# Kernel tuning notes

Measured on AMD Instinct MI355X. Metric: run time of the kernel, lower is better.

Reference implementation:

```python
import jax, jax.numpy as jnp
import numpy as np

B, S, H = 16, 1024, 1024
MAX_SIMS = 100
K_FOCUS = 3  # min(3, seq_len)
SIM_OPTIONS = jnp.array([10, 25, 50, 75, 100], dtype=jnp.int32)


def _gelu(x):
    return jax.nn.gelu(x, approximate=False)  # torch nn.GELU default = exact erf


def _mlp(x, W1, b1, W2, b2):
    return _gelu(x @ W1 + b1) @ W2 + b2


def setup_inputs() -> dict:
    key = jax.random.key(0)
    ks = jax.random.split(key, 24)
    sc = 0.02
    d = {
        'hidden_states': jax.random.normal(ks[0], (B, S, H), dtype=jnp.float32),
        'attention_mask': jnp.ones((B, S), dtype=jnp.int32),
        # simulation_controller: Linear(H,H) -> GELU -> Linear(H,5)
        'Wsc1': jax.random.normal(ks[1], (H, H)) * sc, 'bsc1': jnp.zeros((H,)),
        'Wsc2': jax.random.normal(ks[2], (H, 5)) * sc, 'bsc2': jnp.zeros((5,)),
        # policy: Linear(H,H) -> GELU -> Linear(H,H)
        'Wp1': jax.random.normal(ks[3], (H, H)) * sc, 'bp1': jnp.zeros((H,)),
        'Wp2': jax.random.normal(ks[4], (H, H)) * sc, 'bp2': jnp.zeros((H,)),
        # transition: Linear(2H,H) -> GELU -> (Dropout eval=identity) -> Linear(H,H)
        'Wt1': jax.random.normal(ks[5], (2 * H, H)) * sc, 'bt1': jnp.zeros((H,)),
        'Wt2': jax.random.normal(ks[6], (H, H)) * sc, 'bt2': jnp.zeros((H,)),
        # action_value: Linear(2H,H) -> GELU -> Linear(H,1)
        'Wav1': jax.random.normal(ks[7], (2 * H, H)) * sc, 'bav1': jnp.zeros((H,)),
        'Wav2': jax.random.normal(ks[8], (H, 1)) * sc, 'bav2': jnp.zeros((1,)),
        # aggregation: Linear(2H,H) -> GELU -> Linear(H,H)
        'Wg1': jax.random.normal(ks[9], (2 * H, H)) * sc, 'bg1': jnp.zeros((H,)),
        'Wg2': jax.random.normal(ks[10], (H, H)) * sc, 'bg2': jnp.zeros((H,)),
    }
    return d


def reference(hidden_states, attention_mask,
              Wsc1, bsc1, Wsc2, bsc2,
              Wp1, bp1, Wp2, bp2,
              Wt1, bt1, Wt2, bt2,
              Wav1, bav1, Wav2, bav2,
              Wg1, bg1, Wg2, bg2):
    b, s, h = hidden_states.shape
    root = hidden_states
    # eval-mode sim count selection: argmax over controller logits
    sim_logits = _mlp(root[:, 0], Wsc1, bsc1, Wsc2, bsc2)          # [B,5]
    sims = SIM_OPTIONS[jnp.argmax(sim_logits, axis=-1)]            # [B]

    policy_scores = _mlp(root, Wp1, bp1, Wp2, bp2)                 # [B,S,H]
    focus_logits = policy_scores.mean(axis=-1)                     # [B,S]
    focus_logits = jnp.where(attention_mask == 0, -1e9, focus_logits)
    root_mean = root.mean(axis=1)                                  # [B,H]
    brange = jnp.arange(b)
    base_key = jax.random.key(42)

    def step(acc, t):
        k = jax.random.fold_in(base_key, t)
        # multinomial without replacement via Gumbel top-k on the logits
        g = jax.random.gumbel(k, (b, s), dtype=focus_logits.dtype)
        _, focus_pos = jax.lax.top_k(focus_logits + g, K_FOCUS)    # [B,3]
        focus_states = jnp.take_along_axis(root, focus_pos[:, :, None], axis=1)  # [B,3,H]
        current = root
        for j in range(K_FOCUS):
            trans_in = jnp.concatenate([current.mean(axis=1), focus_states[:, j]], axis=-1)  # [B,2H]
            new_state = _mlp(trans_in, Wt1, bt1, Wt2, bt2)         # [B,H]
            current = current.at[brange, focus_pos[:, j]].set(new_state)
        value = _mlp(jnp.concatenate([root_mean, current.mean(axis=1)], axis=-1),
                     Wav1, bav1, Wav2, bav2)                       # [B,1]
        w = jax.nn.sigmoid(value)[:, :, None]                      # [B,1,1]
        active = (t < sims).astype(current.dtype)[:, None, None]   # mask sims beyond per-example count
        return acc + active * w * current, None

    acc, _ = jax.lax.scan(step, root, jnp.arange(MAX_SIMS))
    enhanced = _mlp(jnp.concatenate([root, acc], axis=-1), Wg1, bg1, Wg2, bg2)
    return hidden_states + enhanced
```

## Files before the change

kernel.cpp:

```cpp
#include <hip/hip_runtime.h>
#include <hip/hip_bf16.h>
#include <cstdint>
#include <math.h>


#define SEQ 1024
#define BATCH 16
#define HDIM 1024
#define NSIM 100
#define NCHAIN (NSIM * BATCH)
#define NCH3 (3 * NCHAIN)
#define SHC (SEQ * HDIM)

typedef short bf16x8 __attribute__((ext_vector_type(8)));
typedef float f32x4 __attribute__((ext_vector_type(4)));
typedef float float4v __attribute__((ext_vector_type(4)));

__device__ __forceinline__ unsigned short f2bf(float f) {
    union { float f; uint32_t u; } c; c.f = f;
    uint32_t u = c.u;
    return (unsigned short)((u + 0x7FFFu + ((u >> 16) & 1u)) >> 16);
}
__device__ __forceinline__ float bf2f(unsigned short h) {
    union { uint32_t u; float f; } c; c.u = ((uint32_t)h) << 16;
    return c.f;
}

__device__ __forceinline__ void gll16(const void* g, void* l) {
    __builtin_amdgcn_global_load_lds(
        (const __attribute__((address_space(1))) void*)g,
        (__attribute__((address_space(3))) void*)l, 16, 0, 0);
}

__device__ __forceinline__ float gelu32(float x) {
    return 0.5f * x * (1.0f + erff(x * 0.70710678f));
}

__device__ __forceinline__ void swz_block(int& bx, int& by) {
    int gx = gridDim.x;
    int h = blockIdx.y * gx + blockIdx.x;
    int nwg = gx * gridDim.y;
    int l = (h & 7) * (nwg >> 3) + (h >> 3);
    bx = l % gx; by = l / gx;
}

__device__ __forceinline__ uint32_t rotl32(uint32_t v, int r) {
    return (v << r) | (v >> (32 - r));
}

__device__ __forceinline__ void threefry(uint32_t k0, uint32_t k1,
                                         uint32_t c0, uint32_t c1,
                                         uint32_t& o0, uint32_t& o1) {
    uint32_t ks0 = k0, ks1 = k1, ks2 = k0 ^ k1 ^ 0x1BD11BDAu;
    uint32_t x0 = c0 + ks0, x1 = c1 + ks1;
#define TFR(r) { x0 += x1; x1 = rotl32(x1, r); x1 ^= x0; }
    TFR(13) TFR(15) TFR(26) TFR(6)   x0 += ks1; x1 += ks2 + 1u;
    TFR(17) TFR(29) TFR(16) TFR(24)  x0 += ks2; x1 += ks0 + 2u;
    TFR(13) TFR(15) TFR(26) TFR(6)   x0 += ks0; x1 += ks1 + 3u;
    TFR(17) TFR(29) TFR(16) TFR(24)  x0 += ks1; x1 += ks2 + 4u;
    TFR(13) TFR(15) TFR(26) TFR(6)   x0 += ks2; x1 += ks0 + 5u;
#undef TFR
    o0 = x0; o1 = x1;
}

__device__ __forceinline__ bool better(float va, int ia, float vb, int ib) {
    return (va > vb) || (va == vb && ia < ib);
}

__global__ __launch_bounds__(256)
void transpose_bf16(const float* __restrict__ W, unsigned short* __restrict__ WT,
                    int K, int N) {
    __shared__ float t[32][33];
    int kb = blockIdx.x * 32, nb = blockIdx.y * 32;
    int tx = threadIdx.x & 31, ty4 = threadIdx.x >> 5;
#pragma unroll
    for (int p = 0; p < 4; ++p) {
        int ky = ty4 + p * 8;
        t[ky][tx] = W[(long)(kb + ky) * N + nb + tx];
    }
    __syncthreads();
#pragma unroll
    for (int p = 0; p < 4; ++p) {
        int ny = ty4 + p * 8;
        WT[(long)(nb + ny) * K + kb + tx] = f2bf(t[tx][ny]);
    }
}

__global__ __launch_bounds__(256)
void transpose_split3(const float* __restrict__ W, unsigned short* __restrict__ WT3,
                      int K, int N) {
    __shared__ float t[32][33];
    int kb = blockIdx.x * 32, nb = blockIdx.y * 32;
    int tx = threadIdx.x & 31, ty4 = threadIdx.x >> 5;
#pragma unroll
    for (int p = 0; p < 4; ++p) {
        int ky = ty4 + p * 8;
        t[ky][tx] = W[(long)(kb + ky) * N + nb + tx];
    }
    __syncthreads();
#pragma unroll
    for (int p = 0; p < 4; ++p) {
        int ny = ty4 + p * 8;
        float w = t[tx][ny];
        unsigned short h = f2bf(w);
        unsigned short l = f2bf(w - bf2f(h));
        long base = (long)(nb + ny) * 3072;
        WT3[base + kb + tx] = h;
        WT3[base + 1024 + kb + tx] = l;
        WT3[base + 2048 + kb + tx] = h;
    }
}

__global__ __launch_bounds__(256)
void cvt_split(const float* __restrict__ src, unsigned short* __restrict__ hi,
               unsigned short* __restrict__ lo, long n8) {
    long i = (long)blockIdx.x * 256 + threadIdx.x;
    long stride = (long)gridDim.x * 256;
    for (; i < n8; i += stride) {
        const float* s = src + i * 8;
        float4v v0 = *(const float4v*)s;
        float4v v1 = *(const float4v*)(s + 4);
        bf16x8 h, l;
#pragma unroll
        for (int e = 0; e < 4; ++e) {
            unsigned short h0 = f2bf(v0[e]);
            h[e] = (short)h0;
            unsigned short h1 = f2bf(v1[e]);
            h[e + 4] = (short)h1;
            if (lo) {
                l[e] = (short)f2bf(v0[e] - bf2f(h0));
                l[e + 4] = (short)f2bf(v1[e] - bf2f(h1));
            }
        }
        *(bf16x8*)&hi[i * 8] = h;
        if (lo) *(bf16x8*)&lo[i * 8] = l;
    }
}

__global__ __launch_bounds__(256)
void rv2_kernel(const float* __restrict__ rmean, const float* __restrict__ W,
                float* __restrict__ Rv) {
    int blk = blockIdx.x;
    int b = blk >> 5, nc = (blk >> 3) & 3, kc = blk & 7;
    int n = (nc << 8) + threadIdx.x;
    float s = 0.f;
    int k0 = kc << 7;
    for (int k = k0; k < k0 + 128; ++k)
        s = fmaf(rmean[b * 1024 + k], W[(long)k * 1024 + n], s);
    atomicAdd(&Rv[b * 1024 + n], s);
}

__global__ __launch_bounds__(256)
void rootmean_part(const float* __restrict__ root, double* __restrict__ part) {
    int b = blockIdx.x >> 4, sc = blockIdx.x & 15;
#pragma unroll
    for (int hp = 0; hp < 4; ++hp) {
        int h = (hp << 8) + threadIdx.x;
        const float* base = root + (size_t)b * SHC + ((size_t)sc << 16) + h;
        double s = 0.0;
        for (int ss = 0; ss < 64; ++ss) s += (double)base[(size_t)ss << 10];
        part[(((long)b << 4) + sc) * 1024 + h] = s;
    }
}
__global__ void rootmean_fin(const double* __restrict__ part, float* __restrict__ rmean,
                             unsigned short* __restrict__ rmean_bf) {
    int e = blockIdx.x * 256 + threadIdx.x;
    int b = e >> 10, h = e & 1023;
    double s = 0.0;
    for (int sc = 0; sc < 16; ++sc) s += part[(((long)b << 4) + sc) * 1024 + h];
    float v = (float)(s * (1.0 / 1024.0));
    rmean[e] = v;
    rmean_bf[e] = f2bf(v);
}

template<int TM, int TN, int BK, int EPI>
__global__ __launch_bounds__(512)
void gemm_bt(const unsigned short* __restrict__ Av1, long lda1, const int* __restrict__ a1rows,
             const unsigned short* __restrict__ Av2, long lda2, const int* __restrict__ a2rows,
             int K1, int kmod1,
             const unsigned short* __restrict__ WT,
             const float* __restrict__ bias,
             const float* __restrict__ wp2m, double* __restrict__ fl64,
             const float* __restrict__ Pre,
             const float* __restrict__ Cadd,
             float* __restrict__ C,
             unsigned short* __restrict__ Cbf,
             long ldc, int M, int N, int K, int doGelu) {
    constexpr int MT = TM / 32;
    constexpr int NT = TN / 64;
    constexpr int WROWS = TM / 2;
    constexpr int WCOLS = TN / 4;
    constexpr int CH = BK / 8;
    constexpr int ASLOT = TM * CH;
    constexpr int BSLOT = TN * CH;
    __shared__ unsigned short As[2][TM * BK];
    __shared__ unsigned short Bs[2][TN * BK];
    __shared__ int r1s[TM], r2s[TM];
    int tid = threadIdx.x;
    int bx, by; swz_block(bx, by);
    int row0 = by * TM, col0 = bx * TN;
    if (tid < TM) {
        int gm = row0 + tid; if (gm >= M) gm = M - 1;
        r1s[tid] = a1rows ? a1rows[gm] : gm;
        r2s[tid] = a2rows ? a2rows[gm] : gm;
    }
    int wid = tid >> 6, lane = tid & 63;
    int wr = wid >> 2, wc = wid & 3;
    int llo = lane & 15, lhi = lane >> 4;
    auto swzc = [](int cs, int r) -> int {
        if constexpr (BK == 64) return cs ^ (r & 7);
        else                    return cs ^ ((r >> 1) & 3);
    };
    f32x4 acc[MT][NT];
#pragma unroll
    for (int i = 0; i < MT; i++)
#pragma unroll
        for (int j = 0; j < NT; j++) acc[i][j] = (f32x4){0.f, 0.f, 0.f, 0.f};
    __syncthreads();

    auto stage = [&](int k0, int b) {
#pragma unroll
        for (int i = 0; i < (BSLOT + 511) / 512; ++i) {
            int q = tid + (i << 9);
            if (BSLOT % 512 == 0 || q < BSLOT) {
                int r = q / CH, cs = q % CH, c = swzc(cs, r);
                gll16(WT + (long)(col0 + r) * K + (k0 + (c << 3)),
                      (char*)Bs[b] + (q << 4));
            }
        }
        bool s1 = (k0 < K1);
        const unsigned short* Ab = s1 ? Av1 : Av2;
        const int* rsel = s1 ? r1s : r2s;
        long lda = s1 ? lda1 : lda2;
        int kb = s1 ? (k0 & kmod1) : (k0 - K1);
#pragma unroll
        for (int i = 0; i < (ASLOT + 511) / 512; ++i) {
            int q = tid + (i << 9);
            if (ASLOT % 512 == 0 || q < ASLOT) {
                int r = q / CH, cs = q % CH, c = swzc(cs, r);
                gll16(Ab + (long)rsel[r] * lda + (kb + (c << 3)),
                      (char*)As[b] + (q << 4));
            }
        }
    };

    stage(0, 0);
    int nIt = K / BK;
    for (int it = 0; it < nIt; ++it) {
        int cur = it & 1;
        __syncthreads();
        if (it + 1 < nIt) stage((it + 1) * BK, cur ^ 1);
        __builtin_amdgcn_sched_barrier(0);
        char* AsB = (char*)As[cur];
        char* BsB = (char*)Bs[cur];
#pragma unroll
        for (int ks = 0; ks < BK / 32; ++ks) {
            bf16x8 af[MT], bfv[NT];
#pragma unroll
            for (int mt = 0; mt < MT; ++mt) {
                int r = wr * WROWS + mt * 16 + llo;
                int pc = swzc((ks << 2) | lhi, r);
                af[mt] = *(const bf16x8*)(AsB + ((r * CH + pc) << 4));
            }
#pragma unroll
            for (int nt = 0; nt < NT; ++nt) {
                int r = wc * WCOLS + nt * 16 + llo;
                int pc = swzc((ks << 2) | lhi, r);
                bfv[nt] = *(const bf16x8*)(BsB + ((r * CH + pc) << 4));
            }
#pragma unroll
            for (int mt = 0; mt < MT; ++mt)
#pragma unroll
                for (int nt = 0; nt < NT; ++nt)
                    acc[mt][nt] = __builtin_amdgcn_mfma_f32_16x16x32_bf16(
                        af[mt], bfv[nt], acc[mt][nt], 0, 0, 0);
        }
    }
    if constexpr (EPI == 0) {
#pragma unroll
        for (int mt = 0; mt < MT; ++mt) {
#pragma unroll
            for (int nt = 0; nt < NT; ++nt) {
                int gn = col0 + wc * WCOLS + nt * 16 + llo;
#pragma unroll
                for (int r = 0; r < 4; ++r) {
                    int rl = wr * WROWS + mt * 16 + lhi * 4 + r;
                    int gm = row0 + rl;
                    if (gm >= M) continue;
                    float v = acc[mt][nt][r] + bias[gn];
                    if (Pre) v += Pre[(long)r2s[rl] * 1024 + gn];
                    if (doGelu) v = gelu32(v);
                    if (Cadd) v += Cadd[(long)gm * ldc + gn];
                    if (C)   C[(long)gm * ldc + gn] = v;
                    if (Cbf) Cbf[(long)gm * ldc + gn] = f2bf(v);
                }
            }
        }
    } else {
#pragma unroll
        for (int mt = 0; mt < MT; ++mt) {
            double part[4] = {0.0, 0.0, 0.0, 0.0};
#pragma unroll
            for (int nt = 0; nt < NT; ++nt) {
                int gn = col0 + wc * WCOLS + nt * 16 + llo;
                float b = bias[gn], wn = wp2m[gn];
#pragma unroll
                for (int r = 0; r < 4; ++r) {
                    float x = acc[mt][nt][r] + b;
                    part[r] += (double)gelu32(x) * (double)wn;
                }
            }
#pragma unroll
            for (int r = 0; r < 4; ++r) {
                double v = part[r];
                v += __shfl_xor(v, 1);
                v += __shfl_xor(v, 2);
                v += __shfl_xor(v, 4);
                v += __shfl_xor(v, 8);
                if (llo == 0)
                    atomicAdd(&fl64[row0 + wr * WROWS + mt * 16 + lhi * 4 + r], v);
            }
        }
    }
}

__global__ void flbuild_kernel(const double* __restrict__ fl64,
                               const float* __restrict__ wp2m,
                               const int* __restrict__ amask,
                               float* __restrict__ fl32) {
    int m = blockIdx.x * 256 + threadIdx.x;
    fl32[m] = (amask[m] == 0) ? -1e9f : (float)(fl64[m] + (double)wp2m[1024]);
}

__global__ void wp2mean_kernel(const float* __restrict__ Wp2,
                               const float* __restrict__ bp2,
                               float* __restrict__ outv) {
    __shared__ double sb[256];
    int r = blockIdx.x, tid = threadIdx.x;
    const float* src = (r < 1024) ? (Wp2 + (size_t)r * 1024) : bp2;
    double s = 0.0;
    for (int k = tid; k < 1024; k += 256) s += (double)src[k];
    sb[tid] = s; __syncthreads();
    for (int off = 128; off > 0; off >>= 1) {
        if (tid < off) sb[tid] += sb[tid + off];
        __syncthreads();
    }
    if (tid == 0) outv[r] = (float)(sb[0] * (1.0 / 1024.0));
}

__global__ __launch_bounds__(256)
void ctrl_fc1(const float* __restrict__ root, const float* __restrict__ W,
              const float* __restrict__ b1, float* __restrict__ T1) {
    __shared__ double red[16][17];
    int ni = threadIdx.x & 15, kt = threadIdx.x >> 4;
    int n = blockIdx.x * 16 + ni;
    double accb[16];
#pragma unroll
    for (int bb = 0; bb < 16; ++bb) accb[bb] = 0.0;
    for (int k = kt * 64; k < kt * 64 + 64; ++k) {
        double w = (double)W[(long)k * 1024 + n];
#pragma unroll
        for (int bb = 0; bb < 16; ++bb)
            accb[bb] = fma((double)root[(long)bb * SHC + k], w, accb[bb]);
    }
    for (int bb = 0; bb < 16; ++bb) {
        red[kt][ni] = accb[bb];
        __syncthreads();
        if (kt == 0) {
            double s = 0.0;
            for (int q = 0; q < 16; ++q) s += red[q][ni];
            double x = s + (double)b1[n];
            T1[bb * 1024 + n] = (float)(0.5 * x * (1.0 + erf(x * 0.70710678118654752440)));
        }
        __syncthreads();
    }
}

__global__ void ctrl_fc2(const float* __restrict__ T1, const float* __restrict__ W2,
                         const float* __restrict__ b2, float* __restrict__ logits) {
    __shared__ double sb[256];
    int bn = blockIdx.x;
    int b = bn / 5, n = bn % 5;
    double s = 0.0;
    for (int k = threadIdx.x; k < 1024; k += 256)
        s += (double)T1[b * 1024 + k] * (double)W2[k * 5 + n];
    sb[threadIdx.x] = s; __syncthreads();
    for (int off = 128; off > 0; off >>= 1) {
        if (threadIdx.x < off) sb[threadIdx.x] += sb[threadIdx.x + off];
        __syncthreads();
    }
    if (threadIdx.x == 0) logits[b * 5 + n] = (float)(sb[0] + (double)b2[n]);
}

__global__ void sims_kernel(const float* __restrict__ logits, int* __restrict__ sims) {
    int b = threadIdx.x;
    if (b >= BATCH) return;
    float best = logits[b * 5 + 0]; int biv = 0;
    for (int i = 1; i < 5; i++) {
        float v = logits[b * 5 + i];
        if (v > best) { best = v; biv = i; }
    }
    const int opt[5] = {10, 25, 50, 75, 100};
    sims[b] = opt[biv];
}

__global__ void gumbel_kernel(const float* __restrict__ fl,
                              int* __restrict__ idxj, int* __restrict__ vidx) {
    __shared__ float sv[256][3];
    __shared__ int   si[256][3];
    int blk = blockIdx.x;
    int t = blk >> 4, b = blk & 15;
    uint32_t kk0, kk1;
    threefry(0u, 42u, 0u, (uint32_t)t, kk0, kk1);
    int tid = threadIdx.x;
    float bv[3] = {-INFINITY, -INFINITY, -INFINITY};
    int   bi[3] = {0x7FFFFFFF, 0x7FFFFFFF, 0x7FFFFFFF};
    for (int s = tid; s < SEQ; s += 256) {
        uint32_t m = (uint32_t)(b * SEQ + s);
        uint32_t y0, y1;
        threefry(kk0, kk1, 0u, m, y0, y1);
        uint32_t bits = y0 ^ y1;
        float f = __uint_as_float((bits >> 9) | 0x3F800000u) - 1.0f;
        float u = fmaxf(1.17549435e-38f, f);
        float l1 = (float)log((double)u);
        float l2 = (float)log(-(double)l1);
        float g  = -l2;
        float val = fl[b * SEQ + s] + g;
        if (better(val, s, bv[2], bi[2])) {
            bv[2] = val; bi[2] = s;
            if (better(bv[2], bi[2], bv[1], bi[1])) {
                float tv = bv[1]; int ti = bi[1];
                bv[1] = bv[2]; bi[1] = bi[2]; bv[2] = tv; bi[2] = ti;
            }
            if (better(bv[1], bi[1], bv[0], bi[0])) {
                float tv = bv[0]; int ti = bi[0];
                bv[0] = bv[1]; bi[0] = bi[1]; bv[1] = tv; bi[1] = ti;
            }
        }
    }
    sv[tid][0] = bv[0]; sv[tid][1] = bv[1]; sv[tid][2] = bv[2];
    si[tid][0] = bi[0]; si[tid][1] = bi[1]; si[tid][2] = bi[2];
    __syncthreads();
    for (int off = 128; off > 0; off >>= 1) {
        if (tid < off) {
            float av[3] = {sv[tid][0], sv[tid][1], sv[tid][2]};
            int   ai[3] = {si[tid][0], si[tid][1], si[tid][2]};
            float cv[3] = {sv[tid + off][0], sv[tid + off][1], sv[tid + off][2]};
            int   ci[3] = {si[tid + off][0], si[tid + off][1], si[tid + off][2]};
            float rv[3]; int ri[3]; int pa = 0, pb = 0;
#pragma unroll
            for (int r = 0; r < 3; r++) {
                if (better(av[pa], ai[pa], cv[pb], ci[pb])) { rv[r] = av[pa]; ri[r] = ai[pa]; pa++; }
                else                                        { rv[r] = cv[pb]; ri[r] = ci[pb]; pb++; }
            }
            sv[tid][0] = rv[0]; sv[tid][1] = rv[1]; sv[tid][2] = rv[2];
            si[tid][0] = ri[0]; si[tid][1] = ri[1]; si[tid][2] = ri[2];
        }
        __syncthreads();
    }
    if (tid == 0) {
        idxj[0 * NCHAIN + blk] = b * SEQ + si[0][0];
        idxj[1 * NCHAIN + blk] = b * SEQ + si[0][1];
        idxj[2 * NCHAIN + blk] = b * SEQ + si[0][2];
        vidx[blk] = b;
    }
}

__global__ void vidx3_kernel(int* __restrict__ vidx3) {
    int m = blockIdx.x * 256 + threadIdx.x;
    if (m < NCH3) vidx3[m] = m & 15;
}

__global__ void meanfinal_kernel(const float* __restrict__ rmean,
                                 const float* __restrict__ NS,
                                 const float* __restrict__ root,
                                 const int* __restrict__ idxj,
                                 unsigned short* __restrict__ mc_bf) {
    int e = blockIdx.x * 256 + threadIdx.x;
    int c = e >> 10, hh = e & 1023;
    double m = (double)rmean[(c & 15) * HDIM + hh];
#pragma unroll
    for (int j = 0; j < 3; ++j) {
        int r = idxj[j * NCHAIN + c];
        m += ((double)NS[((long)j * NCHAIN + c) * 1024 + hh] -
              (double)root[(long)r * 1024 + hh]) * (1.0 / 1024.0);
    }
    mc_bf[e] = f2bf((float)m);
}

__global__ void valdot_kernel(const float* __restrict__ HV, const float* __restrict__ Wav2,
                              const float* __restrict__ bav2, float* __restrict__ w) {
    __shared__ double sb[256];
    int c = blockIdx.x, tid = threadIdx.x;
    double s = 0.0;
    for (int k = tid; k < HDIM; k += 256) s += (double)HV[(size_t)c * HDIM + k] * (double)Wav2[k];
    sb[tid] = s; __syncthreads();
    for (int off = 128; off > 0; off >>= 1) {
        if (tid < off) sb[tid] += sb[tid + off];
        __syncthreads();
    }
    if (tid == 0) {
        double v = sb[0] + (double)bav2[0];
        w[c] = (float)(1.0 / (1.0 + exp(-v)));
    }
}

__global__ void wsum_kernel(const float* __restrict__ w, const int* __restrict__ sims,
                            double* __restrict__ Wsum) {
    int b = threadIdx.x;
    if (b >= BATCH) return;
    int sb = sims[b];
    double s = 0.0;
    for (int t = 0; t < sb; t++) s += (double)w[t * BATCH + b];
    Wsum[b] = s;
}

__global__ void accinit_kernel(const float* __restrict__ root, const double* __restrict__ Wsum,
                               float* __restrict__ acc) {
    size_t e = (size_t)blockIdx.x * 256 + threadIdx.x;
    int b = (int)(e >> 20);
    acc[e] = (float)((1.0 + Wsum[b]) * (double)root[e]);
}

__global__ __launch_bounds__(256)
void corrections_atomic(const float* __restrict__ NS, const float* __restrict__ root,
                        const float* __restrict__ w, const int* __restrict__ sims,
                        const int* __restrict__ idxj, float* __restrict__ acc) {
    int blk = blockIdx.x;
    int j = blk / NCHAIN, c = blk % NCHAIN;
    int b = c & 15, t = c >> 4;
    if (t >= sims[b]) return;
    float wv = w[c];
    int row = idxj[j * NCHAIN + c];
    const float* ns = NS + ((long)j * NCHAIN + c) * 1024;
    const float* rt = root + (long)row * 1024;
    float* ac = acc + (long)row * 1024;
    for (int h = threadIdx.x; h < 1024; h += 256)
        atomicAdd(&ac[h], wv * (ns[h] - rt[h]));
}

extern "C" void kernel_launch(void* const* d_in, const int* in_sizes, int n_in,
                              void* d_out, int out_size, void* d_ws, size_t ws_size,
                              hipStream_t stream) {
    (void)in_sizes; (void)n_in; (void)out_size; (void)ws_size;
    const float* root = (const float*)d_in[0];
    const int*   amask = (const int*)d_in[1];
    const float* Wsc1 = (const float*)d_in[2];  const float* bsc1 = (const float*)d_in[3];
    const float* Wsc2 = (const float*)d_in[4];  const float* bsc2 = (const float*)d_in[5];
    const float* Wp1  = (const float*)d_in[6];  const float* bp1  = (const float*)d_in[7];
    const float* Wp2  = (const float*)d_in[8];  const float* bp2  = (const float*)d_in[9];
    const float* Wt1  = (const float*)d_in[10]; const float* bt1  = (const float*)d_in[11];
    const float* Wt2  = (const float*)d_in[12]; const float* bt2  = (const float*)d_in[13];
    const float* Wav1 = (const float*)d_in[14]; const float* bav1 = (const float*)d_in[15];
    const float* Wav2 = (const float*)d_in[16]; const float* bav2 = (const float*)d_in[17];
    const float* Wg1  = (const float*)d_in[18]; const float* bg1  = (const float*)d_in[19];
    const float* Wg2  = (const float*)d_in[20]; const float* bg2  = (const float*)d_in[21];
    float* out = (float*)d_out;

    char* p = (char*)d_ws;
    auto carve = [&](size_t nbytes) -> void* {
        void* r = (void*)p; p += (nbytes + 255) & ~(size_t)255; return r;
    };
    unsigned short* H1big = (unsigned short*)carve((size_t)NCH3 * HDIM * 2);
    float*          Hav   = (float*)carve((size_t)NCHAIN * HDIM * 4);
    float*          NS    = (float*)carve((size_t)3 * NCHAIN * HDIM * 4);
    unsigned short* h_bf  = (unsigned short*)H1big;
    unsigned short* WT3   = (unsigned short*)NS;
    unsigned short* WTt1  = (unsigned short*)carve((size_t)1024 * 1024 * 2);
    unsigned short* WTt2  = (unsigned short*)carve((size_t)1024 * 1024 * 2);
    unsigned short* WTav1 = (unsigned short*)carve((size_t)1024 * 1024 * 2);
    unsigned short* WTg1  = (unsigned short*)carve((size_t)1024 * 2048 * 2);
    unsigned short* WTg2  = (unsigned short*)carve((size_t)1024 * 1024 * 2);
    float*  rmean  = (float*)carve(BATCH * HDIM * 4);
    float*  Rv_t   = (float*)carve(BATCH * HDIM * 4);
    float*  Rv_av  = (float*)carve(BATCH * HDIM * 4);
    double* rpart  = (double*)carve((size_t)BATCH * 16 * HDIM * 8);
    float*  T1     = (float*)carve(BATCH * HDIM * 4);
    float*  logits = (float*)carve(128 * 4);
    float*  wp2m   = (float*)carve(1040 * 4);
    double* fl64   = (double*)carve((size_t)BATCH * SEQ * 8);
    float*  fl32   = (float*)carve(BATCH * SEQ * 4);
    float*  wbuf   = (float*)carve(NCHAIN * 4);
    double* Wsumd  = (double*)carve(64 * 8);
    int*    sims   = (int*)carve(64 * 4);
    int*    idxj   = (int*)carve(3 * NCHAIN * 4);
    int*    vidx   = (int*)carve(NCHAIN * 4);
    int*    vidx3  = (int*)carve(NCH3 * 4);
    unsigned short* root_bf     = (unsigned short*)carve((size_t)BATCH * SEQ * HDIM * 2);
    unsigned short* acc_bf      = (unsigned short*)carve((size_t)BATCH * SEQ * HDIM * 2);
    unsigned short* root_lo     = acc_bf;
    unsigned short* mean_cur_bf = (unsigned short*)carve((size_t)NCHAIN * HDIM * 2);
    unsigned short* rmean_bf    = (unsigned short*)carve(BATCH * HDIM * 2);

    const long NTOT8 = (long)BATCH * SEQ * HDIM / 8;
    const int  KBIG = 1 << 30, KMA = 0x7FFFFFFF;

    transpose_bf16<<<dim3(1024 / 32, 1024 / 32), 256, 0, stream>>>(
        Wt1 + (size_t)1024 * 1024, WTt1, 1024, 1024);
    transpose_bf16<<<dim3(1024 / 32, 1024 / 32), 256, 0, stream>>>(Wt2, WTt2, 1024, 1024);
    transpose_bf16<<<dim3(1024 / 32, 1024 / 32), 256, 0, stream>>>(
        Wav1 + (size_t)1024 * 1024, WTav1, 1024, 1024);
    transpose_bf16<<<dim3(2048 / 32, 1024 / 32), 256, 0, stream>>>(Wg1, WTg1, 2048, 1024);
    transpose_bf16<<<dim3(1024 / 32, 1024 / 32), 256, 0, stream>>>(Wg2, WTg2, 1024, 1024);
    transpose_split3<<<dim3(32, 32), 256, 0, stream>>>(Wp1, WT3, 1024, 1024);
    cvt_split<<<2048, 256, 0, stream>>>(root, root_bf, root_lo, NTOT8);
    vidx3_kernel<<<(NCH3 + 255) / 256, 256, 0, stream>>>(vidx3);
    hipMemsetAsync(Rv_t, 0, BATCH * HDIM * 4, stream);
    hipMemsetAsync(Rv_av, 0, BATCH * HDIM * 4, stream);
    wp2mean_kernel<<<1025, 256, 0, stream>>>(Wp2, bp2, wp2m);
    rootmean_part<<<256, 256, 0, stream>>>(root, rpart);
    rootmean_fin<<<64, 256, 0, stream>>>(rpart, rmean, rmean_bf);
    rv2_kernel<<<512, 256, 0, stream>>>(rmean, Wt1, Rv_t);
    rv2_kernel<<<512, 256, 0, stream>>>(rmean, Wav1, Rv_av);
    ctrl_fc1<<<64, 256, 0, stream>>>(root, Wsc1, bsc1, T1);
    ctrl_fc2<<<80, 256, 0, stream>>>(T1, Wsc2, bsc2, logits);
    sims_kernel<<<1, 64, 0, stream>>>(logits, sims);
    hipMemsetAsync(fl64, 0, (size_t)BATCH * SEQ * 8, stream);
    gemm_bt<128, 256, 32, 1><<<dim3(4, 128), 512, 0, stream>>>(
        root_bf, 1024, nullptr, root_lo, 1024, nullptr, 2048, 1023,
        WT3, bp1, wp2m, fl64, nullptr, nullptr, nullptr, nullptr, 1024,
        BATCH * SEQ, 1024, 3072, 0);
    flbuild_kernel<<<BATCH * SEQ / 256, 256, 0, stream>>>(fl64, wp2m, amask, fl32);
    gumbel_kernel<<<NCHAIN, 256, 0, stream>>>(fl32, idxj, vidx);
    gemm_bt<64, 128, 64, 0><<<dim3(8, 75), 512, 0, stream>>>(
        root_bf, 1024, idxj, nullptr, 0, vidx3, KBIG, KMA,
        WTt1, bt1, nullptr, nullptr, Rv_t, nullptr, nullptr, H1big, 1024,
        NCH3, 1024, 1024, 1);
    gemm_bt<64, 128, 64, 0><<<dim3(8, 75), 512, 0, stream>>>(
        H1big, 1024, nullptr, nullptr, 0, nullptr, KBIG, KMA,
        WTt2, bt2, nullptr, nullptr, nullptr, nullptr, NS, nullptr,
        1024, NCH3, 1024, 1024, 0);
    meanfinal_kernel<<<NCHAIN * HDIM / 256, 256, 0, stream>>>(
        rmean, NS, root, idxj, mean_cur_bf);
    gemm_bt<64, 128, 64, 0><<<dim3(8, 25), 512, 0, stream>>>(
        mean_cur_bf, 1024, nullptr, nullptr, 0, vidx, KBIG, KMA,
        WTav1, bav1, nullptr, nullptr, Rv_av, nullptr, Hav, nullptr, 1024,
        NCHAIN, 1024, 1024, 1);
    valdot_kernel<<<NCHAIN, 256, 0, stream>>>(Hav, Wav2, bav2, wbuf);
    wsum_kernel<<<1, 64, 0, stream>>>(wbuf, sims, Wsumd);
    accinit_kernel<<<(BATCH * SEQ * HDIM) / 256, 256, 0, stream>>>(root, Wsumd, out);
    corrections_atomic<<<3 * NCHAIN, 256, 0, stream>>>(NS, root, wbuf, sims, idxj, out);
    cvt_split<<<2048, 256, 0, stream>>>(out, acc_bf, nullptr, NTOT8);
    gemm_bt<128, 256, 32, 0><<<dim3(4, 128), 512, 0, stream>>>(
        root_bf, 1024, nullptr, acc_bf, 1024, nullptr, 1024, KMA,
        WTg1, bg1, nullptr, nullptr, nullptr, nullptr, nullptr, h_bf, 1024,
        BATCH * SEQ, 1024, 2048, 1);
    gemm_bt<128, 256, 32, 0><<<dim3(4, 128), 512, 0, stream>>>(
        h_bf, 1024, nullptr, nullptr, 0, nullptr, KBIG, KMA,
        WTg2, bg2, nullptr, nullptr, nullptr, root, out, nullptr, 1024,
        BATCH * SEQ, 1024, 1024, 0);
}
```

Before: 614.9 us.

## Triple-buffer GEMM staging with vmcnt waits and fuse bf16 conversion into accinit

```diff
diff --git a/kernel.cpp b/kernel.cpp
--- a/kernel.cpp
+++ b/kernel.cpp
@@ -193,8 +193,10 @@
     constexpr int CH = BK / 8;
     constexpr int ASLOT = TM * CH;
     constexpr int BSLOT = TN * CH;
-    __shared__ unsigned short As[2][TM * BK];
-    __shared__ unsigned short Bs[2][TN * BK];
+    static_assert(ASLOT % 512 == 0 && BSLOT % 512 == 0, "full-thread staging");
+    static_assert(ASLOT / 512 + BSLOT / 512 == 3, "G must be 3 for vmcnt(3)");
+    __shared__ unsigned short As[3][TM * BK];
+    __shared__ unsigned short Bs[3][TN * BK];
     __shared__ int r1s[TM], r2s[TM];
     int tid = threadIdx.x;
     int bx, by; swz_block(bx, by);
@@ -220,13 +222,11 @@
 
     auto stage = [&](int k0, int b) {
 #pragma unroll
-        for (int i = 0; i < (BSLOT + 511) / 512; ++i) {
+        for (int i = 0; i < BSLOT / 512; ++i) {
             int q = tid + (i << 9);
-            if (BSLOT % 512 == 0 || q < BSLOT) {
-                int r = q / CH, cs = q % CH, c = swzc(cs, r);
-                gll16(WT + (long)(col0 + r) * K + (k0 + (c << 3)),
-                      (char*)Bs[b] + (q << 4));
-            }
+            int r = q / CH, cs = q % CH, c = swzc(cs, r);
+            gll16(WT + (long)(col0 + r) * K + (k0 + (c << 3)),
+                  (char*)Bs[b] + (q << 4));
         }
         bool s1 = (k0 < K1);
         const unsigned short* Ab = s1 ? Av1 : Av2;
@@ -234,23 +234,27 @@
         long lda = s1 ? lda1 : lda2;
         int kb = s1 ? (k0 & kmod1) : (k0 - K1);
 #pragma unroll
-        for (int i = 0; i < (ASLOT + 511) / 512; ++i) {
+        for (int i = 0; i < ASLOT / 512; ++i) {
             int q = tid + (i << 9);
-            if (ASLOT % 512 == 0 || q < ASLOT) {
-                int r = q / CH, cs = q % CH, c = swzc(cs, r);
-                gll16(Ab + (long)rsel[r] * lda + (kb + (c << 3)),
-                      (char*)As[b] + (q << 4));
-            }
+            int r = q / CH, cs = q % CH, c = swzc(cs, r);
+            gll16(Ab + (long)rsel[r] * lda + (kb + (c << 3)),
+                  (char*)As[b] + (q << 4));
         }
     };
 
+    int nIt = K / BK;
     stage(0, 0);
-    int nIt = K / BK;
+    if (nIt > 1) stage(BK, 1);
     for (int it = 0; it < nIt; ++it) {
-        int cur = it & 1;
-        __syncthreads();
-        if (it + 1 < nIt) stage((it + 1) * BK, cur ^ 1);
+        int cur = it % 3;
+        if (it + 1 < nIt) {
+            asm volatile("s_waitcnt vmcnt(3)" ::: "memory");
+        } else {
+            asm volatile("s_waitcnt vmcnt(0)" ::: "memory");
+        }
+        __builtin_amdgcn_s_barrier();
         __builtin_amdgcn_sched_barrier(0);
+        if (it + 2 < nIt) stage((it + 2) * BK, (it + 2) % 3);
         char* AsB = (char*)As[cur];
         char* BsB = (char*)Bs[cur];
 #pragma unroll
@@ -515,11 +519,15 @@
     Wsum[b] = s;
 }
 
-__global__ void accinit_kernel(const float* __restrict__ root, const double* __restrict__ Wsum,
-                               float* __restrict__ acc) {
+__global__ void accinit2_kernel(const float* __restrict__ root,
+                                const double* __restrict__ Wsum,
+                                float* __restrict__ acc,
+                                unsigned short* __restrict__ acc_bf) {
     size_t e = (size_t)blockIdx.x * 256 + threadIdx.x;
     int b = (int)(e >> 20);
-    acc[e] = (float)((1.0 + Wsum[b]) * (double)root[e]);
+    float v = (float)((1.0 + Wsum[b]) * (double)root[e]);
+    acc[e] = v;
+    acc_bf[e] = f2bf(v);
 }
 
 __global__ __launch_bounds__(256)
@@ -537,6 +545,16 @@
     float* ac = acc + (long)row * 1024;
     for (int h = threadIdx.x; h < 1024; h += 256)
         atomicAdd(&ac[h], wv * (ns[h] - rt[h]));
+}
+
+__global__ __launch_bounds__(256)
+void reconv_kernel(const float* __restrict__ acc, const int* __restrict__ idxj,
+                   unsigned short* __restrict__ acc_bf) {
+    int row = idxj[blockIdx.x];
+    const float* src = acc + (long)row * 1024;
+    unsigned short* dst = acc_bf + (long)row * 1024;
+    for (int h = threadIdx.x; h < 1024; h += 256)
+        dst[h] = f2bf(src[h]);
 }
 
 extern "C" void kernel_launch(void* const* d_in, const int* in_sizes, int n_in,
@@ -638,9 +656,10 @@
         NCHAIN, 1024, 1024, 1);
     valdot_kernel<<<NCHAIN, 256, 0, stream>>>(Hav, Wav2, bav2, wbuf);
     wsum_kernel<<<1, 64, 0, stream>>>(wbuf, sims, Wsumd);
-    accinit_kernel<<<(BATCH * SEQ * HDIM) / 256, 256, 0, stream>>>(root, Wsumd, out);
+    accinit2_kernel<<<(BATCH * SEQ * HDIM) / 256, 256, 0, stream>>>(
+        root, Wsumd, out, acc_bf);
     corrections_atomic<<<3 * NCHAIN, 256, 0, stream>>>(NS, root, wbuf, sims, idxj, out);
-    cvt_split<<<2048, 256, 0, stream>>>(out, acc_bf, nullptr, NTOT8);
+    reconv_kernel<<<NCH3, 256, 0, stream>>>(out, idxj, acc_bf);
     gemm_bt<128, 256, 32, 0><<<dim3(4, 128), 512, 0, stream>>>(
         root_bf, 1024, nullptr, acc_bf, 1024, nullptr, 1024, KMA,
         WTg1, bg1, nullptr, nullptr, nullptr, nullptr, nullptr, h_bf, 1024,
```

Measured after the change: 639.0 us. +3.9%, slower.
